# Optimization experiments

Hardware: AMD Instinct MI355X
Metric: run time of the kernel (lower is better)

The kernel has to match this reference:

```python
import jax, jax.numpy as jnp
import numpy as np


def setup_inputs() -> dict:
    key = jax.random.key(0)
    ks = jax.random.split(key, 5)
    B, N, Fin, Fout = 8, 2048, 512, 512
    stdv = 1.0 / np.sqrt(Fout)
    w_stdv = 1.0 / np.sqrt(Fin)
    x = jax.random.normal(ks[0], (B, N, Fin), dtype=jnp.float32)
    weight = jax.random.uniform(ks[1], (Fin, Fout), dtype=jnp.float32, minval=-stdv, maxval=stdv)
    bias = jax.random.uniform(ks[2], (Fout,), dtype=jnp.float32, minval=-stdv, maxval=stdv)
    w_one = jax.random.uniform(ks[3], (Fin, Fin), dtype=jnp.float32, minval=-w_stdv, maxval=w_stdv)
    w_two = jax.random.uniform(ks[4], (Fin, Fin), dtype=jnp.float32, minval=-w_stdv, maxval=w_stdv)
    return {"x": x, "weight": weight, "bias": bias, "w_one": w_one, "w_two": w_two}


def reference(x, weight, bias, w_one, w_two):
    # x: [B, N, Fin]
    support = jnp.einsum('bnf,fo->bno', x, weight)          # [B, N, Fout]
    phi_one = jnp.einsum('ef,bnf->ben', w_one, x)           # [B, Fin, N]
    phi_two = jnp.einsum('ef,bnf->ben', w_two, x)           # [B, Fin, N]
    adj = jnp.einsum('ben,bem->bnm', phi_one, phi_two)      # [B, N, N]
    adj = jax.nn.softmax(adj, axis=1)                        # softmax over dim=1 (columns)
    out = jnp.einsum('bnm,bmo->bno', adj, support)           # [B, N, Fout]
    return out + bias
```

## Files before the change

kernel.cpp:

```cpp
#include <hip/hip_runtime.h>
#include <math.h>

#define BB 8
#define NN 2048
#define FF 512
#define LOG2E 1.4426950408889634f

typedef __attribute__((ext_vector_type(8))) short short8;
typedef __attribute__((ext_vector_type(4))) float floatx4;
typedef __attribute__((ext_vector_type(2))) float float2v;
typedef __attribute__((ext_vector_type(2))) __bf16 bf16x2;

__device__ __forceinline__ unsigned short f2bf(float f) {
    union { float f; unsigned u; } v; v.f = f;
    unsigned r = v.u + 0x7FFFu + ((v.u >> 16) & 1u);
    return (unsigned short)(r >> 16);
}

__device__ __forceinline__ float fexp2(float x) {
#if __has_builtin(__builtin_amdgcn_exp2f)
    return __builtin_amdgcn_exp2f(x);
#else
    return __expf(x * 0.69314718056f);
#endif
}

#define SB0() __builtin_amdgcn_sched_barrier(0)
#define BARRIER() do { SB0(); asm volatile("s_barrier" ::: "memory"); SB0(); } while (0)
#define GLDS(src, dst) __builtin_amdgcn_global_load_lds( \
    (const __attribute__((address_space(1))) void*)(src), \
    (__attribute__((address_space(3))) void*)(dst), 16, 0, 0)
#define VMW(n) asm volatile("s_waitcnt vmcnt(" #n ")" ::: "memory")

template<int M_REP, int MODE>
__global__ __launch_bounds__(256, 1) void gemm8p(
    const unsigned short* __restrict__ A, const unsigned short* __restrict__ B,
    void* __restrict__ Cv, const float* __restrict__ bias, float* __restrict__ Dsum,
    int K, int a_ld, int b_ld, int ldc,
    long a_batch, long b_batch, long c_batch)
{
    constexpr int BM    = M_REP * 32;
    constexpr int LA    = BM / 64;
    constexpr int ASLOT = BM * 32;
    constexpr int BSLOT = 256 * 32;
    constexpr int BBASE = 4 * ASLOT;
    constexpr int TOT   = 4 * ASLOT + 4 * BSLOT;

    __shared__ __align__(16) unsigned short SH[TOT];

    const int tid  = threadIdx.x;
    const int wave = tid >> 6;
    const int lane = tid & 63;
    const int wr   = wave >> 1;
    const int wc   = wave & 1;
    const int fl   = lane & 15;
    const int quad = lane >> 4;

    const int gx = gridDim.x, gy = gridDim.y;
    int flat = blockIdx.x + gx * (blockIdx.y + gy * blockIdx.z);
    const int cpx = (gx * gy * gridDim.z) >> 3;
    flat = (flat & 7) * cpx + (flat >> 3);
    const int bx = flat % gx;
    const int rest = flat / gx;
    const int by = rest % gy;
    const int bz = rest / gy;

    const int m0 = by * BM;
    const int n0 = bx * 256;

    const unsigned short* Aptr = A + (long)bz * a_batch + (long)m0 * a_ld;
    const unsigned short* Bptr = B + (long)bz * b_batch + (long)n0 * b_ld;

    int offA[LA], offB[4];
    #pragma unroll
    for (int i = 0; i < LA; ++i) {
        const int cl = i * 256 + tid;
        const int r = cl >> 2, s = cl & 3;
        offA[i] = r * a_ld + (s ^ ((r >> 1) & 3)) * 8;
    }
    #pragma unroll
    for (int i = 0; i < 4; ++i) {
        const int cl = i * 256 + tid;
        const int r = cl >> 2, s = cl & 3;
        offB[i] = r * b_ld + (s ^ ((r >> 1) & 3)) * 8;
    }

    const int swz = (quad ^ ((fl >> 1) & 3)) * 8;
    const int aRd = (wr * (M_REP * 16) + fl) * 32 + swz;
    const int bRd = (wc * 128 + fl) * 32 + swz;

    auto sA = [&](int kh, int db, int kb) {
        #pragma unroll
        for (int i = 0; i < LA; ++i)
            GLDS(Aptr + kb + offA[i], &SH[(kh * 2 + db) * ASLOT + (i * 256 + tid) * 8]);
    };
    auto sB = [&](int kh, int db, int kb) {
        #pragma unroll
        for (int i = 0; i < 4; ++i)
            GLDS(Bptr + kb + offB[i], &SH[BBASE + (kh * 2 + db) * BSLOT + (i * 256 + tid) * 8]);
    };

    floatx4 acc[M_REP][8] = {};
    short8 afA[M_REP], afB[M_REP], bfA[4], bfB[4];

    auto RA = [&](short8* af, int kh, int db) {
        const unsigned short* b = &SH[(kh * 2 + db) * ASLOT + aRd];
        #pragma unroll
        for (int m = 0; m < M_REP; ++m) af[m] = *(const short8*)(b + m * 512);
    };
    auto RB = [&](short8* bf, int kh, int db, int nh) {
        const unsigned short* b = &SH[BBASE + (kh * 2 + db) * BSLOT + bRd + nh * 2048];
        #pragma unroll
        for (int j = 0; j < 4; ++j) bf[j] = *(const short8*)(b + j * 512);
    };
    auto MC = [&](short8* af, short8* bf, int nh) {
        __builtin_amdgcn_s_setprio(1);
        #pragma unroll
        for (int m = 0; m < M_REP; ++m)
            #pragma unroll
            for (int j = 0; j < 4; ++j)
                acc[m][nh * 4 + j] = __builtin_amdgcn_mfma_f32_16x16x32_bf16(af[m], bf[j], acc[m][nh * 4 + j], 0, 0, 0);
        __builtin_amdgcn_s_setprio(0);
    };

    const int nt = K >> 6;
    const int ni = nt >> 1;

    sA(0, 0, 0);  sB(0, 0, 0);  sA(1, 0, 32); sB(1, 0, 32);
    sA(0, 1, 64); sB(0, 1, 64); sA(1, 1, 96);
    if constexpr (M_REP == 8) VMW(12); else VMW(8);
    BARRIER();
    RA(afA, 0, 0); RB(bfA, 0, 0, 0);
    SB0();

    for (int i = 0; i < ni; ++i) {
        const bool last = (i == ni - 1);
        const int kb1 = (2 * i + 1) * 64, kb2 = kb1 + 64, kb3 = kb2 + 64;

        sB(1, 1, kb1 + 32);
        BARRIER();
        RB(bfB, 0, 0, 1); SB0();
        MC(afA, bfA, 0);
        BARRIER();
        if (!last) sA(0, 0, kb2);
        BARRIER();
        RA(afB, 1, 0); RB(bfA, 1, 0, 0); SB0();
        MC(afA, bfB, 1);
        BARRIER();
        if (!last) sB(0, 0, kb2);
        BARRIER();
        RB(bfB, 1, 0, 1); SB0();
        MC(afB, bfA, 0);
        BARRIER();
        if (!last) {
            sA(1, 0, kb2 + 32);
            if constexpr (M_REP == 8) VMW(12); else VMW(8);
        } else {
            VMW(0);
        }
        BARRIER();
        RA(afA, 0, 1); RB(bfA, 0, 1, 0); SB0();
        MC(afB, bfB, 1);
        BARRIER();
        if (!last) sB(1, 0, kb2 + 32);
        BARRIER();
        RB(bfB, 0, 1, 1); SB0();
        MC(afA, bfA, 0);
        BARRIER();
        if (!last) sA(0, 1, kb3);
        BARRIER();
        RA(afB, 1, 1); RB(bfA, 1, 1, 0); SB0();
        MC(afA, bfB, 1);
        BARRIER();
        if (!last) sB(0, 1, kb3);
        BARRIER();
        RB(bfB, 1, 1, 1); SB0();
        MC(afB, bfA, 0);
        BARRIER();
        if (!last) {
            sA(1, 1, kb3 + 32);
            if constexpr (M_REP == 8) VMW(12); else VMW(8);
        }
        BARRIER();
        if (!last) { RA(afA, 0, 0); RB(bfA, 0, 0, 0); }
        SB0();
        MC(afB, bfB, 1);
        BARRIER();
    }

    const int wmg = m0 + wr * (M_REP * 16);
    const int wcol = wc * 128;

    if constexpr (MODE == 0) {
        float* Cb = (float*)Cv + (long)bz * c_batch;
        #pragma unroll
        for (int n = 0; n < 8; ++n) {
            const int ng = n0 + wcol + n * 16 + fl;
            const float badd = bias ? bias[ng] : 0.0f;
            #pragma unroll
            for (int m = 0; m < M_REP; ++m) {
                const int mg = wmg + m * 16 + quad * 4;
                #pragma unroll
                for (int r = 0; r < 4; ++r)
                    Cb[(long)(mg + r) * ldc + ng] = acc[m][n][r] + badd;
            }
        }
    } else {
        unsigned short* Cb = (unsigned short*)Cv + (long)bz * c_batch;
        if constexpr (MODE == 2) {
            float* Db = Dsum + (long)bz * NN;
            #pragma unroll
            for (int m = 0; m < M_REP; ++m)
                #pragma unroll
                for (int n = 0; n < 8; ++n)
                    #pragma unroll
                    for (int r = 0; r < 4; ++r)
                        acc[m][n][r] = fexp2(acc[m][n][r]);
            #pragma unroll
            for (int n = 0; n < 8; ++n) {
                float csum = 0.f;
                #pragma unroll
                for (int m = 0; m < M_REP; ++m)
                    csum += acc[m][n][0] + acc[m][n][1] + acc[m][n][2] + acc[m][n][3];
                csum += __shfl_xor(csum, 16);
                csum += __shfl_xor(csum, 32);
                if (quad == 0) atomicAdd(&Db[n0 + wcol + n * 16 + fl], csum);
            }
        }
        __syncthreads();
        #pragma unroll
        for (int m = 0; m < M_REP; ++m) {
            const int rowb = wr * (M_REP * 16) + m * 16 + quad * 4;
            #pragma unroll
            for (int n = 0; n < 8; ++n) {
                const int pc = (wcol + n * 16 + fl) ^ (quad << 4);
                #pragma unroll
                for (int r = 0; r < 4; ++r)
                    SH[(rowb + r) * 256 + pc] = f2bf(acc[m][n][r]);
            }
        }
        __syncthreads();
        #pragma unroll
        for (int k = 0; k < BM / 8; ++k) {
            const int idx = k * 256 + tid;
            const int row = idx >> 5, c8 = (idx & 31) * 8;
            const int lcol = c8 ^ (((row >> 2) & 3) << 4);
            short8 vv = *(const short8*)&SH[row * 256 + lcol];
            *(short8*)&Cb[(long)(m0 + row) * ldc + n0 + c8] = vv;
        }
    }
}

__global__ __launch_bounds__(256) void convert_all(
    const float* __restrict__ x, const float* __restrict__ w1, const float* __restrict__ w2,
    unsigned short* __restrict__ xb, unsigned short* __restrict__ w1b, unsigned short* __restrict__ w2b)
{
    const long NX = (long)BB * NN * FF / 8;
    const long NW = (long)FF * FF / 8;
    long t = (long)blockIdx.x * 256 + threadIdx.x;
    const float* in; unsigned short* out; float sc = 1.0f;
    if (t < NX) { in = x; out = xb; }
    else if (t < NX + NW) { in = w1; out = w1b; t -= NX; sc = LOG2E; }
    else if (t < NX + 2 * NW) { in = w2; out = w2b; t -= NX + NW; }
    else return;
    const long i = t * 8;
    float4 a = *(const float4*)(in + i);
    float4 b = *(const float4*)(in + i + 4);
    union { bf16x2 h[4]; short8 s8; } u;
    float2v v;
    v.x = a.x * sc; v.y = a.y * sc; u.h[0] = __builtin_convertvector(v, bf16x2);
    v.x = a.z * sc; v.y = a.w * sc; u.h[1] = __builtin_convertvector(v, bf16x2);
    v.x = b.x * sc; v.y = b.y * sc; u.h[2] = __builtin_convertvector(v, bf16x2);
    v.x = b.z * sc; v.y = b.w * sc; u.h[3] = __builtin_convertvector(v, bf16x2);
    *(short8*)(out + i) = u.s8;
}

__global__ __launch_bounds__(256) void transpose_convert(
    const float* __restrict__ in, unsigned short* __restrict__ out, int dim)
{
    __shared__ float t[32][33];
    const int tx = threadIdx.x & 31, ty = threadIdx.x >> 5;
    const int x0 = blockIdx.x * 32, y0 = blockIdx.y * 32;
    #pragma unroll
    for (int k = 0; k < 32; k += 8)
        t[ty + k][tx] = in[(long)(y0 + ty + k) * dim + x0 + tx];
    __syncthreads();
    #pragma unroll
    for (int k = 0; k < 32; k += 8)
        out[(long)(x0 + ty + k) * dim + y0 + tx] = f2bf(t[tx][ty + k]);
}

__global__ __launch_bounds__(256) void zero_f32(float* __restrict__ p, long n)
{
    long i = (long)blockIdx.x * 256 + threadIdx.x;
    if (i < n) p[i] = 0.0f;
}

__global__ __launch_bounds__(256) void scale_transpose(
    const unsigned short* __restrict__ Call, const float* __restrict__ D,
    unsigned short* __restrict__ supT, int batch0)
{
    __shared__ float t[32][33];
    __shared__ float rD[32];
    const int tx = threadIdx.x & 31, ty = threadIdx.x >> 5;
    const int mt = blockIdx.x * 32, ot = blockIdx.y * 32;
    const int b = batch0 + blockIdx.z;
    const unsigned short* Cb = Call + (long)b * NN * 1536;
    unsigned short* Tb = supT + (long)b * NN * FF;
    if (threadIdx.x < 32) rD[threadIdx.x] = 1.0f / D[(long)b * NN + mt + threadIdx.x];
    __syncthreads();
    #pragma unroll
    for (int k = 0; k < 32; k += 8) {
        unsigned short u = Cb[(long)(mt + ty + k) * 1536 + 1024 + ot + tx];
        union { unsigned uu; float f; } cv; cv.uu = ((unsigned)u) << 16;
        t[ty + k][tx] = cv.f;
    }
    __syncthreads();
    #pragma unroll
    for (int k = 0; k < 32; k += 8)
        Tb[(long)(ot + ty + k) * NN + mt + tx] = f2bf(t[tx][ty + k] * rD[tx]);
}

extern "C" void kernel_launch(void* const* d_in, const int* in_sizes, int n_in,
                              void* d_out, int out_size, void* d_ws, size_t ws_size,
                              hipStream_t stream)
{
    const float* x      = (const float*)d_in[0];
    const float* weight = (const float*)d_in[1];
    const float* bias   = (const float*)d_in[2];
    const float* w_one  = (const float*)d_in[3];
    const float* w_two  = (const float*)d_in[4];
    float* out = (float*)d_out;

    const long NF  = (long)NN * FF;
    const long NN2 = (long)NN * NN;
    const long CROW = 1536;

    char* p = (char*)d_ws;
    unsigned short* xb    = (unsigned short*)p; p += (size_t)BB * NF * 2;
    unsigned short* Wall  = (unsigned short*)p; p += (size_t)CROW * FF * 2;
    unsigned short* Call  = (unsigned short*)p; p += (size_t)BB * NN * CROW * 2;
    unsigned short* supT  = (unsigned short*)p; p += (size_t)BB * NF * 2;
    float*          Dsum  = (float*)p;          p += (size_t)BB * NN * 4;
    unsigned short* E     = (unsigned short*)p;
    unsigned short* w1b = Wall;
    unsigned short* w2b = Wall + (size_t)FF * FF;
    unsigned short* wTb = Wall + (size_t)2 * FF * FF;

    const size_t fixed = (size_t)(p - (char*)d_ws);
    const bool full = ws_size >= fixed + (size_t)BB * NN2 * 2;

    dim3 blk(256);

    convert_all<<<dim3(4352), blk, 0, stream>>>(x, w_one, w_two, xb, w1b, w2b);
    transpose_convert<<<dim3(FF / 32, FF / 32), blk, 0, stream>>>(weight, wTb, FF);
    zero_f32<<<dim3((BB * NN) / 256), blk, 0, stream>>>(Dsum, BB * NN);

    gemm8p<4, 1><<<dim3(CROW / 256, NN / 128, BB), blk, 0, stream>>>(
        xb, Wall, Call, nullptr, nullptr, FF,
        FF, FF, (int)CROW, NF, 0, NN * CROW);

    if (full) {
        gemm8p<8, 2><<<dim3(NN / 256, NN / 256, BB), blk, 0, stream>>>(
            Call, Call + FF, E, nullptr, Dsum, FF,
            (int)CROW, (int)CROW, NN, NN * CROW, NN * CROW, NN2);
        scale_transpose<<<dim3(NN / 32, FF / 32, BB), blk, 0, stream>>>(Call, Dsum, supT, 0);
        gemm8p<4, 0><<<dim3(FF / 256, NN / 128, BB), blk, 0, stream>>>(
            E, supT, out, bias, nullptr, NN,
            NN, NN, FF, NN2, NF, NF);
    } else {
        for (int b = 0; b < BB; ++b) {
            const unsigned short* Cb = Call + (size_t)b * NN * CROW;
            gemm8p<8, 2><<<dim3(NN / 256, NN / 256, 1), blk, 0, stream>>>(
                Cb, Cb + FF, E, nullptr, Dsum + (size_t)b * NN, FF,
                (int)CROW, (int)CROW, NN, 0, 0, 0);
            scale_transpose<<<dim3(NN / 32, FF / 32, 1), blk, 0, stream>>>(Call, Dsum, supT, b);
            gemm8p<4, 0><<<dim3(FF / 256, NN / 128, 1), blk, 0, stream>>>(
                E, supT + (size_t)b * NF, out + (size_t)b * NF, bias, nullptr, NN,
                NN, NN, FF, 0, 0, 0);
        }
    }
}
```

Baseline: 239.4 us.

## Replace GEMM with 512-thread 256x256 tile kernel using 8 waves

Replaces the templated 256-thread GEMM (128 or 256 row tiles) with a single 512-thread kernel that always computes 256x256 tiles, spread over 8 waves in a 2x4 layout. The main loop changes from a register double-buffered fragment schedule to one that loads fragments and then waits on lgkmcnt before each MFMA group, with plain s_barrier calls. The aim is more waves per CU to hide latency and larger tiles for the first and last GEMMs, which also halves their grid size. The cost is less LDS-to-register prefetch overlap and fewer blocks in the smaller GEMMs, which risks poor CU fill.

```diff
diff --git a/kernel.cpp b/kernel.cpp
--- a/kernel.cpp
+++ b/kernel.cpp
@@ -25,34 +25,37 @@
 #endif
 }
 
-#define SB0() __builtin_amdgcn_sched_barrier(0)
-#define BARRIER() do { SB0(); asm volatile("s_barrier" ::: "memory"); SB0(); } while (0)
+__device__ __forceinline__ void pk_store(unsigned short* p0, unsigned short* p1,
+                                         float a, float b) {
+    union { bf16x2 h; unsigned short s[2]; } u;
+    float2v v; v.x = a; v.y = b;
+    u.h = __builtin_convertvector(v, bf16x2);
+    *p0 = u.s[0]; *p1 = u.s[1];
+}
+
+#define BAR() __builtin_amdgcn_s_barrier()
+#define LGKM0() do { asm volatile("s_waitcnt lgkmcnt(0)" ::: "memory"); \
+                     __builtin_amdgcn_sched_barrier(0); } while (0)
 #define GLDS(src, dst) __builtin_amdgcn_global_load_lds( \
     (const __attribute__((address_space(1))) void*)(src), \
     (__attribute__((address_space(3))) void*)(dst), 16, 0, 0)
 #define VMW(n) asm volatile("s_waitcnt vmcnt(" #n ")" ::: "memory")
 
-template<int M_REP, int MODE>
-__global__ __launch_bounds__(256, 1) void gemm8p(
+template<int MODE>
+__global__ __launch_bounds__(512) void gemm256(
     const unsigned short* __restrict__ A, const unsigned short* __restrict__ B,
     void* __restrict__ Cv, const float* __restrict__ bias, float* __restrict__ Dsum,
     int K, int a_ld, int b_ld, int ldc,
     long a_batch, long b_batch, long c_batch)
 {
-    constexpr int BM    = M_REP * 32;
-    constexpr int LA    = BM / 64;
-    constexpr int ASLOT = BM * 32;
-    constexpr int BSLOT = 256 * 32;
-    constexpr int BBASE = 4 * ASLOT;
-    constexpr int TOT   = 4 * ASLOT + 4 * BSLOT;
-
-    __shared__ __align__(16) unsigned short SH[TOT];
+    constexpr int SLOT = 256 * 32;
+    __shared__ __align__(16) unsigned short SH[8 * SLOT];
 
     const int tid  = threadIdx.x;
     const int wave = tid >> 6;
     const int lane = tid & 63;
-    const int wr   = wave >> 1;
-    const int wc   = wave & 1;
+    const int wr   = wave >> 2;
+    const int wc   = wave & 3;
     const int fl   = lane & 15;
     const int quad = lane >> 4;
 
@@ -65,61 +68,57 @@
     const int by = rest % gy;
     const int bz = rest / gy;
 
-    const int m0 = by * BM;
+    const int m0 = by * 256;
     const int n0 = bx * 256;
 
     const unsigned short* Aptr = A + (long)bz * a_batch + (long)m0 * a_ld;
     const unsigned short* Bptr = B + (long)bz * b_batch + (long)n0 * b_ld;
 
-    int offA[LA], offB[4];
-    #pragma unroll
-    for (int i = 0; i < LA; ++i) {
-        const int cl = i * 256 + tid;
+    int offA[2], offB[2];
+    #pragma unroll
+    for (int i = 0; i < 2; ++i) {
+        const int cl = i * 512 + tid;
         const int r = cl >> 2, s = cl & 3;
-        offA[i] = r * a_ld + (s ^ ((r >> 1) & 3)) * 8;
-    }
-    #pragma unroll
-    for (int i = 0; i < 4; ++i) {
-        const int cl = i * 256 + tid;
-        const int r = cl >> 2, s = cl & 3;
-        offB[i] = r * b_ld + (s ^ ((r >> 1) & 3)) * 8;
+        const int c = s ^ ((r >> 1) & 3);
+        offA[i] = r * a_ld + c * 8;
+        offB[i] = r * b_ld + c * 8;
     }
 
     const int swz = (quad ^ ((fl >> 1) & 3)) * 8;
-    const int aRd = (wr * (M_REP * 16) + fl) * 32 + swz;
-    const int bRd = (wc * 128 + fl) * 32 + swz;
+    const int aRd = (wr * 128 + fl) * 32 + swz;
+    const int bRd = (wc * 64 + fl) * 32 + swz;
 
     auto sA = [&](int kh, int db, int kb) {
         #pragma unroll
-        for (int i = 0; i < LA; ++i)
-            GLDS(Aptr + kb + offA[i], &SH[(kh * 2 + db) * ASLOT + (i * 256 + tid) * 8]);
+        for (int i = 0; i < 2; ++i)
+            GLDS(Aptr + kb + offA[i], &SH[(kh * 2 + db) * SLOT + (i * 512 + tid) * 8]);
     };
     auto sB = [&](int kh, int db, int kb) {
         #pragma unroll
-        for (int i = 0; i < 4; ++i)
-            GLDS(Bptr + kb + offB[i], &SH[BBASE + (kh * 2 + db) * BSLOT + (i * 256 + tid) * 8]);
-    };
-
-    floatx4 acc[M_REP][8] = {};
-    short8 afA[M_REP], afB[M_REP], bfA[4], bfB[4];
-
-    auto RA = [&](short8* af, int kh, int db) {
-        const unsigned short* b = &SH[(kh * 2 + db) * ASLOT + aRd];
-        #pragma unroll
-        for (int m = 0; m < M_REP; ++m) af[m] = *(const short8*)(b + m * 512);
-    };
-    auto RB = [&](short8* bf, int kh, int db, int nh) {
-        const unsigned short* b = &SH[BBASE + (kh * 2 + db) * BSLOT + bRd + nh * 2048];
-        #pragma unroll
-        for (int j = 0; j < 4; ++j) bf[j] = *(const short8*)(b + j * 512);
-    };
-    auto MC = [&](short8* af, short8* bf, int nh) {
+        for (int i = 0; i < 2; ++i)
+            GLDS(Bptr + kb + offB[i], &SH[(4 + kh * 2 + db) * SLOT + (i * 512 + tid) * 8]);
+    };
+
+    floatx4 acc[8][4] = {};
+    short8 af[8], bf[2];
+
+    auto RA = [&](int kh, int db) {
+        const unsigned short* b = &SH[(kh * 2 + db) * SLOT + aRd];
+        #pragma unroll
+        for (int m = 0; m < 8; ++m) af[m] = *(const short8*)(b + m * 512);
+    };
+    auto RB = [&](int kh, int db, int nh) {
+        const unsigned short* b = &SH[(4 + kh * 2 + db) * SLOT + bRd + nh * 1024];
+        bf[0] = *(const short8*)(b);
+        bf[1] = *(const short8*)(b + 512);
+    };
+    auto MC = [&](int nh) {
         __builtin_amdgcn_s_setprio(1);
         #pragma unroll
-        for (int m = 0; m < M_REP; ++m)
-            #pragma unroll
-            for (int j = 0; j < 4; ++j)
-                acc[m][nh * 4 + j] = __builtin_amdgcn_mfma_f32_16x16x32_bf16(af[m], bf[j], acc[m][nh * 4 + j], 0, 0, 0);
+        for (int m = 0; m < 8; ++m) {
+            acc[m][nh * 2]     = __builtin_amdgcn_mfma_f32_16x16x32_bf16(af[m], bf[0], acc[m][nh * 2], 0, 0, 0);
+            acc[m][nh * 2 + 1] = __builtin_amdgcn_mfma_f32_16x16x32_bf16(af[m], bf[1], acc[m][nh * 2 + 1], 0, 0, 0);
+        }
         __builtin_amdgcn_s_setprio(0);
     };
 
@@ -128,77 +127,51 @@
 
     sA(0, 0, 0);  sB(0, 0, 0);  sA(1, 0, 32); sB(1, 0, 32);
     sA(0, 1, 64); sB(0, 1, 64); sA(1, 1, 96);
-    if constexpr (M_REP == 8) VMW(12); else VMW(8);
-    BARRIER();
-    RA(afA, 0, 0); RB(bfA, 0, 0, 0);
-    SB0();
+    VMW(6);
+    BAR();
 
     for (int i = 0; i < ni; ++i) {
         const bool last = (i == ni - 1);
         const int kb1 = (2 * i + 1) * 64, kb2 = kb1 + 64, kb3 = kb2 + 64;
 
+        RA(0, 0); RB(0, 0, 0);
         sB(1, 1, kb1 + 32);
-        BARRIER();
-        RB(bfB, 0, 0, 1); SB0();
-        MC(afA, bfA, 0);
-        BARRIER();
+        BAR(); LGKM0(); MC(0); BAR();
+        RB(0, 0, 1);
         if (!last) sA(0, 0, kb2);
-        BARRIER();
-        RA(afB, 1, 0); RB(bfA, 1, 0, 0); SB0();
-        MC(afA, bfB, 1);
-        BARRIER();
+        BAR(); LGKM0(); MC(1); BAR();
+        RA(1, 0); RB(1, 0, 0);
         if (!last) sB(0, 0, kb2);
-        BARRIER();
-        RB(bfB, 1, 0, 1); SB0();
-        MC(afB, bfA, 0);
-        BARRIER();
-        if (!last) {
-            sA(1, 0, kb2 + 32);
-            if constexpr (M_REP == 8) VMW(12); else VMW(8);
-        } else {
-            VMW(0);
-        }
-        BARRIER();
-        RA(afA, 0, 1); RB(bfA, 0, 1, 0); SB0();
-        MC(afB, bfB, 1);
-        BARRIER();
+        BAR(); LGKM0(); MC(0); BAR();
+        RB(1, 0, 1);
+        if (!last) { sA(1, 0, kb2 + 32); VMW(6); }
+        else       { VMW(0); }
+        BAR(); LGKM0(); MC(1); BAR();
+        RA(0, 1); RB(0, 1, 0);
         if (!last) sB(1, 0, kb2 + 32);
-        BARRIER();
-        RB(bfB, 0, 1, 1); SB0();
-        MC(afA, bfA, 0);
-        BARRIER();
+        BAR(); LGKM0(); MC(0); BAR();
+        RB(0, 1, 1);
         if (!last) sA(0, 1, kb3);
-        BARRIER();
-        RA(afB, 1, 1); RB(bfA, 1, 1, 0); SB0();
-        MC(afA, bfB, 1);
-        BARRIER();
+        BAR(); LGKM0(); MC(1); BAR();
+        RA(1, 1); RB(1, 1, 0);
         if (!last) sB(0, 1, kb3);
-        BARRIER();
-        RB(bfB, 1, 1, 1); SB0();
-        MC(afB, bfA, 0);
-        BARRIER();
-        if (!last) {
-            sA(1, 1, kb3 + 32);
-            if constexpr (M_REP == 8) VMW(12); else VMW(8);
-        }
-        BARRIER();
-        if (!last) { RA(afA, 0, 0); RB(bfA, 0, 0, 0); }
-        SB0();
-        MC(afB, bfB, 1);
-        BARRIER();
-    }
-
-    const int wmg = m0 + wr * (M_REP * 16);
-    const int wcol = wc * 128;
+        BAR(); LGKM0(); MC(0); BAR();
+        RB(1, 1, 1);
+        if (!last) { sA(1, 1, kb3 + 32); VMW(6); }
+        BAR(); LGKM0(); MC(1); BAR();
+    }
+
+    const int wmg = m0 + wr * 128;
+    const int wcol = wc * 64;
 
     if constexpr (MODE == 0) {
         float* Cb = (float*)Cv + (long)bz * c_batch;
         #pragma unroll
-        for (int n = 0; n < 8; ++n) {
+        for (int n = 0; n < 4; ++n) {
             const int ng = n0 + wcol + n * 16 + fl;
             const float badd = bias ? bias[ng] : 0.0f;
             #pragma unroll
-            for (int m = 0; m < M_REP; ++m) {
+            for (int m = 0; m < 8; ++m) {
                 const int mg = wmg + m * 16 + quad * 4;
                 #pragma unroll
                 for (int r = 0; r < 4; ++r)
@@ -210,17 +183,17 @@
         if constexpr (MODE == 2) {
             float* Db = Dsum + (long)bz * NN;
             #pragma unroll
-            for (int m = 0; m < M_REP; ++m)
+            for (int m = 0; m < 8; ++m)
                 #pragma unroll
-                for (int n = 0; n < 8; ++n)
+                for (int n = 0; n < 4; ++n)
                     #pragma unroll
                     for (int r = 0; r < 4; ++r)
                         acc[m][n][r] = fexp2(acc[m][n][r]);
             #pragma unroll
-            for (int n = 0; n < 8; ++n) {
+            for (int n = 0; n < 4; ++n) {
                 float csum = 0.f;
                 #pragma unroll
-                for (int m = 0; m < M_REP; ++m)
+                for (int m = 0; m < 8; ++m)
                     csum += acc[m][n][0] + acc[m][n][1] + acc[m][n][2] + acc[m][n][3];
                 csum += __shfl_xor(csum, 16);
                 csum += __shfl_xor(csum, 32);
@@ -229,10 +202,10 @@
         }
         __syncthreads();
         #pragma unroll
-        for (int m = 0; m < M_REP; ++m) {
-            const int rowb = wr * (M_REP * 16) + m * 16 + quad * 4;
+        for (int m = 0; m < 8; ++m) {
+            const int rowb = wr * 128 + m * 16 + quad * 4;
             #pragma unroll
-            for (int n = 0; n < 8; ++n) {
+            for (int n = 0; n < 4; ++n) {
                 const int pc = (wcol + n * 16 + fl) ^ (quad << 4);
                 #pragma unroll
                 for (int r = 0; r < 4; ++r)
@@ -241,8 +214,8 @@
         }
         __syncthreads();
         #pragma unroll
-        for (int k = 0; k < BM / 8; ++k) {
-            const int idx = k * 256 + tid;
+        for (int k = 0; k < 16; ++k) {
+            const int idx = k * 512 + tid;
             const int row = idx >> 5, c8 = (idx & 31) * 8;
             const int lcol = c8 ^ (((row >> 2) & 3) << 4);
             short8 vv = *(const short8*)&SH[row * 256 + lcol];
@@ -350,32 +323,32 @@
     const size_t fixed = (size_t)(p - (char*)d_ws);
     const bool full = ws_size >= fixed + (size_t)BB * NN2 * 2;
 
-    dim3 blk(256);
+    dim3 blk(256), blk5(512);
 
     convert_all<<<dim3(4352), blk, 0, stream>>>(x, w_one, w_two, xb, w1b, w2b);
     transpose_convert<<<dim3(FF / 32, FF / 32), blk, 0, stream>>>(weight, wTb, FF);
     zero_f32<<<dim3((BB * NN) / 256), blk, 0, stream>>>(Dsum, BB * NN);
 
-    gemm8p<4, 1><<<dim3(CROW / 256, NN / 128, BB), blk, 0, stream>>>(
+    gemm256<1><<<dim3(CROW / 256, NN / 256, BB), blk5, 0, stream>>>(
         xb, Wall, Call, nullptr, nullptr, FF,
         FF, FF, (int)CROW, NF, 0, NN * CROW);
 
     if (full) {
-        gemm8p<8, 2><<<dim3(NN / 256, NN / 256, BB), blk, 0, stream>>>(
+        gemm256<2><<<dim3(NN / 256, NN / 256, BB), blk5, 0, stream>>>(
             Call, Call + FF, E, nullptr, Dsum, FF,
             (int)CROW, (int)CROW, NN, NN * CROW, NN * CROW, NN2);
         scale_transpose<<<dim3(NN / 32, FF / 32, BB), blk, 0, stream>>>(Call, Dsum, supT, 0);
-        gemm8p<4, 0><<<dim3(FF / 256, NN / 128, BB), blk, 0, stream>>>(
+        gemm256<0><<<dim3(FF / 256, NN / 256, BB), blk5, 0, stream>>>(
             E, supT, out, bias, nullptr, NN,
             NN, NN, FF, NN2, NF, NF);
     } else {
         for (int b = 0; b < BB; ++b) {
             const unsigned short* Cb = Call + (size_t)b * NN * CROW;
-            gemm8p<8, 2><<<dim3(NN / 256, NN / 256, 1), blk, 0, stream>>>(
+            gemm256<2><<<dim3(NN / 256, NN / 256, 1), blk5, 0, stream>>>(
                 Cb, Cb + FF, E, nullptr, Dsum + (size_t)b * NN, FF,
                 (int)CROW, (int)CROW, NN, 0, 0, 0);
             scale_transpose<<<dim3(NN / 32, FF / 32, 1), blk, 0, stream>>>(Call, Dsum, supT, b);
-            gemm8p<4, 0><<<dim3(FF / 256, NN / 128, 1), blk, 0, stream>>>(
+            gemm256<0><<<dim3(FF / 256, NN / 256, 1), blk5, 0, stream>>>(
                 E, supT + (size_t)b * NF, out + (size_t)b * NF, bias, nullptr, NN,
                 NN, NN, FF, 0, 0, 0);
         }
```

New measurement: 235.0 us. About the same (-1.8%).
